# Optimization experiments

Measured on AMD Instinct MI355X. Metric: run time of the kernel, lower is better.

Reference implementation:

```python
import jax, jax.numpy as jnp
import numpy as np

TOP_K = 2

def setup_inputs() -> dict:
    key = jax.random.key(0)
    ks = jax.random.split(key, 5)
    B, S, H, F, E = 4, 512, 1024, 3584, 8
    x = jax.random.normal(ks[0], (B, S, H), dtype=jnp.float32)
    gate_w = jax.random.normal(ks[1], (H, E), dtype=jnp.float32) * (1.0 / np.sqrt(H))
    w1 = jax.random.normal(ks[2], (E, F, H), dtype=jnp.float32) * (1.0 / np.sqrt(H))
    w3 = jax.random.normal(ks[3], (E, F, H), dtype=jnp.float32) * (1.0 / np.sqrt(H))
    w2 = jax.random.normal(ks[4], (E, H, F), dtype=jnp.float32) * (1.0 / np.sqrt(F))
    return {"x": x, "gate_w": gate_w, "w1": w1, "w3": w3, "w2": w2}


def reference(x, gate_w, w1, w3, w2):
    # MoE top-2 routing (Mixtral-style), dense-dispatch formulation.
    B, S, H = x.shape
    E = gate_w.shape[1]
    xt = x.reshape(-1, H)                      # [T, H] flattened tokens
    T = xt.shape[0]
    logits = xt @ gate_w                       # [T, E] gate logits
    top_w, top_i = jax.lax.top_k(logits, TOP_K)    # [T, K]
    top_w = jax.nn.softmax(top_w, axis=-1)         # softmax over selected-k logits
    # combine[t, e] = routing weight of expert e for token t (0 if not selected)
    combine = jnp.zeros((T, E), dtype=xt.dtype)
    combine = combine.at[jnp.arange(T)[:, None], top_i].add(top_w)
    # SwiGLU experts: y_e = w2_e @ (silu(w1_e x) * (w3_e x))
    h = jnp.einsum('th,efh->tef', xt, w1)      # [T, E, F]
    g = jnp.einsum('th,efh->tef', xt, w3)      # [T, E, F]
    act = jax.nn.silu(h) * g                   # [T, E, F]
    out_e = jnp.einsum('tef,ehf->teh', act, w2)  # [T, E, H]
    out = jnp.einsum('teh,te->th', out_e, combine)  # weighted combine over experts
    return out.reshape(B, S, H)
```

## Files before the change

### kernel.cpp

```cpp
#include <hip/hip_runtime.h>
#include <hip/hip_bf16.h>
#include <stdint.h>

#define TOKENS 2048
#define HDIM 1024
#define FDIM 3584
#define NEXP 8
#define BK 32

typedef __attribute__((ext_vector_type(8))) short short8;
typedef __attribute__((ext_vector_type(4))) float floatx4;

#define AS1 __attribute__((address_space(1)))
#define AS3 __attribute__((address_space(3)))

__device__ __forceinline__ void glds16(const void* g, void* l) {
  __builtin_amdgcn_global_load_lds((const AS1 void*)g, (AS3 void*)l, 16, 0, 0);
}

__device__ __forceinline__ unsigned short f2bf(float f) {
  union { float f; unsigned int u; } c; c.f = f;
  unsigned int u = c.u;
  u += 0x7fffu + ((u >> 16) & 1u);
  return (unsigned short)(u >> 16);
}

__device__ __forceinline__ unsigned int pk2bf(float a, float b) {
  __hip_bfloat162 h = __float22bfloat162_rn(make_float2(a, b));
  union { __hip_bfloat162 h; unsigned int u; } c; c.h = h;
  return c.u;
}

__device__ __forceinline__ short8 pack_bf16(float4 c0, float4 c1) {
  union { short8 s; uint4 u; } o;
  o.u.x = pk2bf(c0.x, c0.y); o.u.y = pk2bf(c0.z, c0.w);
  o.u.z = pk2bf(c1.x, c1.y); o.u.w = pk2bf(c1.z, c1.w);
  return o.s;
}

__global__ void gate_kernel(const float* __restrict__ x,
                            const float* __restrict__ gw,
                            int* __restrict__ top_e,
                            float* __restrict__ top_w) {
  int wv = threadIdx.x >> 6;
  int lane = threadIdx.x & 63;
  int t = blockIdx.x * 4 + wv;
  if (t >= TOKENS) return;
  float p[NEXP];
#pragma unroll
  for (int e = 0; e < NEXP; e++) p[e] = 0.f;
  const float* xr = x + (size_t)t * HDIM;
  for (int h = lane; h < HDIM; h += 64) {
    float xv = xr[h];
    const float4* g4 = (const float4*)(gw + (size_t)h * NEXP);
    float4 a = g4[0], b = g4[1];
    p[0] += xv * a.x; p[1] += xv * a.y; p[2] += xv * a.z; p[3] += xv * a.w;
    p[4] += xv * b.x; p[5] += xv * b.y; p[6] += xv * b.z; p[7] += xv * b.w;
  }
#pragma unroll
  for (int e = 0; e < NEXP; e++) {
#pragma unroll
    for (int off = 32; off > 0; off >>= 1) p[e] += __shfl_xor(p[e], off, 64);
  }
  if (lane == 0) {
    int i0 = 0;
    for (int e = 1; e < NEXP; e++) if (p[e] > p[i0]) i0 = e;
    int i1 = (i0 == 0) ? 1 : 0;
    for (int e = 0; e < NEXP; e++) if (e != i0 && p[e] > p[i1]) i1 = e;
    float l0 = p[i0], l1 = p[i1];
    float e1 = __expf(l1 - l0);
    float s = 1.f + e1;
    top_e[t * 2] = i0; top_e[t * 2 + 1] = i1;
    top_w[t * 2] = 1.f / s; top_w[t * 2 + 1] = e1 / s;
  }
}

__global__ void route_kernel(const int* __restrict__ top_e,
                             int* __restrict__ count,
                             int* __restrict__ offs,
                             int* __restrict__ tok_of,
                             int* __restrict__ slot_of) {
  __shared__ int hist[NEXP];
  __shared__ int cur[NEXP];
  int tid = threadIdx.x;
  if (tid < NEXP) hist[tid] = 0;
  __syncthreads();
  int e[4];
#pragma unroll
  for (int j = 0; j < 4; j++) {
    int i = tid * 4 + j;
    e[j] = top_e[i];
    atomicAdd(&hist[e[j]], 1);
  }
  __syncthreads();
  if (tid == 0) {
    int o = 0;
    for (int k = 0; k < NEXP; k++) {
      offs[k] = o; cur[k] = o; count[k] = hist[k]; o += hist[k];
    }
  }
  __syncthreads();
#pragma unroll
  for (int j = 0; j < 4; j++) {
    int i = tid * 4 + j;
    int g = atomicAdd(&cur[e[j]], 1);
    tok_of[g] = i >> 1;
    slot_of[i] = g;
  }
}

__global__ void xconv_kernel(const float* __restrict__ x,
                             unsigned short* __restrict__ xbf) {
  int i = (blockIdx.x * blockDim.x + threadIdx.x) * 4;
  float4 v = *(const float4*)(x + i);
  uint2 pk;
  pk.x = pk2bf(v.x, v.y);
  pk.y = pk2bf(v.z, v.w);
  *(uint2*)(xbf + i) = pk;
}

#define G1_BM 128
#define G1_BF 64

__global__ __launch_bounds__(256, 3)
void gemm1_kernel(const unsigned short* __restrict__ xbf,
                  const float* __restrict__ w1,
                  const float* __restrict__ w3,
                  const int* __restrict__ count,
                  const int* __restrict__ offs,
                  const int* __restrict__ tok_of,
                  unsigned short* __restrict__ act) {
  int e = blockIdx.z;
  int cnt = count[e];
  int m0 = blockIdx.y * G1_BM;
  if (m0 >= cnt) return;
  int f0 = blockIdx.x * G1_BF;
  int off_e = offs[e];

  __shared__ __align__(16) unsigned short sA[2 * G1_BM * 32];
  __shared__ __align__(16) unsigned short sB1[2 * G1_BF * 32];
  __shared__ __align__(16) unsigned short sB3[2 * G1_BF * 32];

  int tid = threadIdx.x;
  int lane = tid & 63, wv = tid >> 6;

  const unsigned short* ag[2];
  char* alb[2];
#pragma unroll
  for (int p = 0; p < 2; p++) {
    int c = tid + p * 256;
    int row = c >> 2, slot = c & 3;
    int gch = slot ^ ((row >> 1) & 3);
    int r = m0 + row;
    int tok = tok_of[off_e + (r < cnt ? r : 0)];
    ag[p] = xbf + (size_t)tok * HDIM + gch * 8;
    alb[p] = (char*)sA + (wv * 64 + p * 256) * 16;
  }
  const float *b1g, *b3g;
  unsigned short *b1l, *b3l;
  {
    int row = tid >> 2, slot = tid & 3;
    int gch = slot ^ ((row >> 1) & 3);
    size_t wrow = (size_t)e * FDIM + f0 + row;
    b1g = w1 + wrow * HDIM + gch * 8;
    b3g = w3 + wrow * HDIM + gch * 8;
    b1l = sB1 + tid * 8;
    b3l = sB3 + tid * 8;
  }

  int lrow = lane & 15, quad = lane >> 4;
  int wm = wv >> 1, wn = wv & 1;

  floatx4 acc1[4][2], acc3[4][2];
#pragma unroll
  for (int i = 0; i < 4; i++)
#pragma unroll
    for (int j = 0; j < 2; j++) {
      acc1[i][j] = (floatx4){0.f, 0.f, 0.f, 0.f};
      acc3[i][j] = (floatx4){0.f, 0.f, 0.f, 0.f};
    }

  const int NT = HDIM / BK;

#pragma unroll
  for (int p = 0; p < 2; p++) glds16(ag[p], alb[p]);
  {
    float4 u0 = *(const float4*)(b1g);
    float4 u1 = *(const float4*)(b1g + 4);
    float4 v0 = *(const float4*)(b3g);
    float4 v1 = *(const float4*)(b3g + 4);
    *(short8*)b1l = pack_bf16(u0, u1);
    *(short8*)b3l = pack_bf16(v0, v1);
  }
  __syncthreads();

  int cur = 0;
  for (int t = 0; t < NT; t++) {
    int nb = cur ^ 1;
    float4 u0, u1, v0, v1;
    if (t + 1 < NT) {
      int k = (t + 1) * BK;
#pragma unroll
      for (int p = 0; p < 2; p++) glds16(ag[p] + k, alb[p] + nb * 8192);
      u0 = *(const float4*)(b1g + k);
      u1 = *(const float4*)(b1g + k + 4);
      v0 = *(const float4*)(b3g + k);
      v1 = *(const float4*)(b3g + k + 4);
    }

    const unsigned short* sAc = sA + cur * (G1_BM * 32);
    const unsigned short* sB1c = sB1 + cur * (G1_BF * 32);
    const unsigned short* sB3c = sB3 + cur * (G1_BF * 32);

    short8 af[4], b1f[2], b3f[2];
#pragma unroll
    for (int ms = 0; ms < 4; ms++) {
      int r = wm * 64 + ms * 16 + lrow;
      int sl = quad ^ ((r >> 1) & 3);
      af[ms] = *(const short8*)(sAc + r * 32 + sl * 8);
    }
#pragma unroll
    for (int ns = 0; ns < 2; ns++) {
      int r = wn * 32 + ns * 16 + lrow;
      int sl = quad ^ ((r >> 1) & 3);
      b1f[ns] = *(const short8*)(sB1c + r * 32 + sl * 8);
      b3f[ns] = *(const short8*)(sB3c + r * 32 + sl * 8);
    }
#pragma unroll
    for (int ms = 0; ms < 4; ms++)
#pragma unroll
      for (int ns = 0; ns < 2; ns++) {
        acc1[ms][ns] = __builtin_amdgcn_mfma_f32_16x16x32_bf16(af[ms], b1f[ns], acc1[ms][ns], 0, 0, 0);
        acc3[ms][ns] = __builtin_amdgcn_mfma_f32_16x16x32_bf16(af[ms], b3f[ns], acc3[ms][ns], 0, 0, 0);
      }

    if (t + 1 < NT) {
      *(short8*)(b1l + nb * (G1_BF * 32)) = pack_bf16(u0, u1);
      *(short8*)(b3l + nb * (G1_BF * 32)) = pack_bf16(v0, v1);
    }
    __syncthreads();
    cur = nb;
  }

#pragma unroll
  for (int ms = 0; ms < 4; ms++) {
#pragma unroll
    for (int reg = 0; reg < 4; reg++) {
      int slot = m0 + wm * 64 + ms * 16 + quad * 4 + reg;
      if (slot < cnt) {
        unsigned short* ar = act + (size_t)(off_e + slot) * FDIM + f0 + wn * 32;
#pragma unroll
        for (int ns = 0; ns < 2; ns++) {
          float h = acc1[ms][ns][reg];
          float g = acc3[ms][ns][reg];
          float a = h / (1.f + __expf(-h)) * g;
          ar[ns * 16 + lrow] = f2bf(a);
        }
      }
    }
  }
}

#define G2_BM 128
#define G2_BN 128
#define SPLITK 2
#define G2_KS (FDIM / SPLITK)

__global__ __launch_bounds__(256, 3)
void gemm2_kernel(const unsigned short* __restrict__ act,
                  const float* __restrict__ w2,
                  const int* __restrict__ count,
                  const int* __restrict__ offs,
                  float* __restrict__ part) {
  int zz = blockIdx.z;
  int e = zz & 7, sk = zz >> 3;
  int cnt = count[e];
  int m0 = blockIdx.y * G2_BM;
  if (m0 >= cnt) return;
  int h0 = blockIdx.x * G2_BN;
  int off_e = offs[e];
  int kb = sk * G2_KS;

  __shared__ __align__(16) unsigned short sA[2 * G2_BM * 32];
  __shared__ __align__(16) unsigned short sB[2 * G2_BN * 32];

  int tid = threadIdx.x;
  int lane = tid & 63, wv = tid >> 6;

  const unsigned short* ag[2];
  char* alb[2];
#pragma unroll
  for (int p = 0; p < 2; p++) {
    int c = tid + p * 256;
    int row = c >> 2, slot = c & 3;
    int gch = slot ^ ((row >> 1) & 3);
    int r = m0 + row;
    int rr = (r < cnt ? r : 0);
    ag[p] = act + (size_t)(off_e + rr) * FDIM + kb + gch * 8;
    alb[p] = (char*)sA + (wv * 64 + p * 256) * 16;
  }
  const float* bg[2];
  unsigned short* bl[2];
#pragma unroll
  for (int p = 0; p < 2; p++) {
    int c = tid + p * 256;
    int row = c >> 2, slot = c & 3;
    int gch = slot ^ ((row >> 1) & 3);
    bg[p] = w2 + ((size_t)e * HDIM + h0 + row) * FDIM + kb + gch * 8;
    bl[p] = sB + c * 8;
  }

  int lrow = lane & 15, quad = lane >> 4;
  int wm = wv >> 1, wn = wv & 1;

  floatx4 acc[4][4];
#pragma unroll
  for (int i = 0; i < 4; i++)
#pragma unroll
    for (int j = 0; j < 4; j++) acc[i][j] = (floatx4){0.f, 0.f, 0.f, 0.f};

  const int NT = G2_KS / BK;

#pragma unroll
  for (int p = 0; p < 2; p++) glds16(ag[p], alb[p]);
#pragma unroll
  for (int p = 0; p < 2; p++) {
    float4 u0 = *(const float4*)(bg[p]);
    float4 u1 = *(const float4*)(bg[p] + 4);
    *(short8*)(bl[p]) = pack_bf16(u0, u1);
  }
  __syncthreads();

  int cur = 0;
  for (int t = 0; t < NT; t++) {
    int nb = cur ^ 1;
    float4 u0[2], u1[2];
    if (t + 1 < NT) {
      int k = (t + 1) * BK;
#pragma unroll
      for (int p = 0; p < 2; p++) glds16(ag[p] + k, alb[p] + nb * 8192);
#pragma unroll
      for (int p = 0; p < 2; p++) {
        u0[p] = *(const float4*)(bg[p] + k);
        u1[p] = *(const float4*)(bg[p] + k + 4);
      }
    }

    const unsigned short* sAc = sA + cur * (G2_BM * 32);
    const unsigned short* sBc = sB + cur * (G2_BN * 32);

    short8 af[4], bf[4];
#pragma unroll
    for (int ms = 0; ms < 4; ms++) {
      int r = wm * 64 + ms * 16 + lrow;
      int sl = quad ^ ((r >> 1) & 3);
      af[ms] = *(const short8*)(sAc + r * 32 + sl * 8);
    }
#pragma unroll
    for (int ns = 0; ns < 4; ns++) {
      int r = wn * 64 + ns * 16 + lrow;
      int sl = quad ^ ((r >> 1) & 3);
      bf[ns] = *(const short8*)(sBc + r * 32 + sl * 8);
    }
#pragma unroll
    for (int ms = 0; ms < 4; ms++)
#pragma unroll
      for (int ns = 0; ns < 4; ns++)
        acc[ms][ns] = __builtin_amdgcn_mfma_f32_16x16x32_bf16(af[ms], bf[ns], acc[ms][ns], 0, 0, 0);

    if (t + 1 < NT) {
#pragma unroll
      for (int p = 0; p < 2; p++)
        *(short8*)(bl[p] + nb * (G2_BN * 32)) = pack_bf16(u0[p], u1[p]);
    }
    __syncthreads();
    cur = nb;
  }

#pragma unroll
  for (int ms = 0; ms < 4; ms++) {
#pragma unroll
    for (int reg = 0; reg < 4; reg++) {
      int slot = m0 + wm * 64 + ms * 16 + quad * 4 + reg;
      if (slot < cnt) {
        float* crow = part + ((size_t)sk * 4096 + off_e + slot) * HDIM + h0 + wn * 64;
#pragma unroll
        for (int ns = 0; ns < 4; ns++)
          crow[ns * 16 + lrow] = acc[ms][ns][reg];
      }
    }
  }
}

__global__ void combine_kernel(const float* __restrict__ part,
                               const int* __restrict__ slot_of,
                               const float* __restrict__ top_w,
                               float* __restrict__ out) {
  int t = blockIdx.x;
  int g0 = slot_of[t * 2], g1 = slot_of[t * 2 + 1];
  float w0 = top_w[t * 2], w1 = top_w[t * 2 + 1];
  int i = threadIdx.x;
  float4 s0 = {0.f, 0.f, 0.f, 0.f}, s1 = {0.f, 0.f, 0.f, 0.f};
#pragma unroll
  for (int sk = 0; sk < SPLITK; sk++) {
    float4 a = ((const float4*)(part + ((size_t)sk * 4096 + g0) * HDIM))[i];
    float4 b = ((const float4*)(part + ((size_t)sk * 4096 + g1) * HDIM))[i];
    s0.x += a.x; s0.y += a.y; s0.z += a.z; s0.w += a.w;
    s1.x += b.x; s1.y += b.y; s1.z += b.z; s1.w += b.w;
  }
  float4 r;
  r.x = w0 * s0.x + w1 * s1.x;
  r.y = w0 * s0.y + w1 * s1.y;
  r.z = w0 * s0.z + w1 * s1.z;
  r.w = w0 * s0.w + w1 * s1.w;
  ((float4*)(out + (size_t)t * HDIM))[i] = r;
}

extern "C" void kernel_launch(void* const* d_in, const int* in_sizes, int n_in,
                              void* d_out, int out_size, void* d_ws, size_t ws_size,
                              hipStream_t stream) {
  const float* x  = (const float*)d_in[0];
  const float* gw = (const float*)d_in[1];
  const float* w1 = (const float*)d_in[2];
  const float* w3 = (const float*)d_in[3];
  const float* w2 = (const float*)d_in[4];
  float* out = (float*)d_out;

  char* ws = (char*)d_ws;
  const size_t MB = 1ull << 20;
  float* top_w = (float*)(ws);
  int* top_e   = (int*)(ws + 16384);
  int* slot_of = (int*)(ws + 32768);
  int* tok_of  = (int*)(ws + 49152);
  int* count   = (int*)(ws + 65536);
  int* offs    = (int*)(ws + 65536 + 64);

  unsigned short* xbf = (unsigned short*)(ws + 1 * MB);
  unsigned short* act = (unsigned short*)(ws + 5 * MB);
  float* part = (float*)(ws + 35 * MB);

  gate_kernel<<<TOKENS / 4, 256, 0, stream>>>(x, gw, top_e, top_w);
  route_kernel<<<1, 1024, 0, stream>>>(top_e, count, offs, tok_of, slot_of);
  xconv_kernel<<<(TOKENS * HDIM) / (256 * 4), 256, 0, stream>>>(x, xbf);
  gemm1_kernel<<<dim3(FDIM / G1_BF, TOKENS / G1_BM, NEXP), 256, 0, stream>>>(
      xbf, w1, w3, count, offs, tok_of, act);
  gemm2_kernel<<<dim3(HDIM / G2_BN, TOKENS / G2_BM, NEXP * SPLITK), 256, 0, stream>>>(
      act, w2, count, offs, part);
  combine_kernel<<<TOKENS, 256, 0, stream>>>(part, slot_of, top_w, out);
}
```

Measured before the change: 508.2 us.

## Fuse x bf16 conversion into gate kernel and deepen B-operand prefetch

The fp32-to-bf16 conversion of x moves into the gate kernel, which already reads x, so one launch and one extra pass over x go away. Both expert GEMMs now prefetch the fp32 weight tile two K-steps ahead in registers and write the next tile's bf16 data to LDS before the MFMA loop instead of after it. This gives global weight loads more time to arrive. It also raises register pressure, which may lower occupancy under the launch bounds.

```diff
diff --git a/kernel.cpp b/kernel.cpp
--- a/kernel.cpp
+++ b/kernel.cpp
@@ -40,6 +40,7 @@
 
 __global__ void gate_kernel(const float* __restrict__ x,
                             const float* __restrict__ gw,
+                            unsigned short* __restrict__ xbf,
                             int* __restrict__ top_e,
                             float* __restrict__ top_w) {
   int wv = threadIdx.x >> 6;
@@ -50,12 +51,24 @@
 #pragma unroll
   for (int e = 0; e < NEXP; e++) p[e] = 0.f;
   const float* xr = x + (size_t)t * HDIM;
-  for (int h = lane; h < HDIM; h += 64) {
-    float xv = xr[h];
-    const float4* g4 = (const float4*)(gw + (size_t)h * NEXP);
-    float4 a = g4[0], b = g4[1];
-    p[0] += xv * a.x; p[1] += xv * a.y; p[2] += xv * a.z; p[3] += xv * a.w;
-    p[4] += xv * b.x; p[5] += xv * b.y; p[6] += xv * b.z; p[7] += xv * b.w;
+  unsigned short* xb = xbf + (size_t)t * HDIM;
+#pragma unroll
+  for (int it = 0; it < 4; it++) {
+    int h = it * 256 + lane * 4;
+    float4 v = *(const float4*)(xr + h);
+    uint2 pk;
+    pk.x = pk2bf(v.x, v.y);
+    pk.y = pk2bf(v.z, v.w);
+    *(uint2*)(xb + h) = pk;
+    const float* g0 = gw + (size_t)h * NEXP;
+#pragma unroll
+    for (int j = 0; j < 4; j++) {
+      float xv = (j == 0) ? v.x : (j == 1) ? v.y : (j == 2) ? v.z : v.w;
+      const float4* g4 = (const float4*)(g0 + j * NEXP);
+      float4 a = g4[0], b = g4[1];
+      p[0] += xv * a.x; p[1] += xv * a.y; p[2] += xv * a.z; p[3] += xv * a.w;
+      p[4] += xv * b.x; p[5] += xv * b.y; p[6] += xv * b.z; p[7] += xv * b.w;
+    }
   }
 #pragma unroll
   for (int e = 0; e < NEXP; e++) {
@@ -107,16 +120,6 @@
     tok_of[g] = i >> 1;
     slot_of[i] = g;
   }
-}
-
-__global__ void xconv_kernel(const float* __restrict__ x,
-                             unsigned short* __restrict__ xbf) {
-  int i = (blockIdx.x * blockDim.x + threadIdx.x) * 4;
-  float4 v = *(const float4*)(x + i);
-  uint2 pk;
-  pk.x = pk2bf(v.x, v.y);
-  pk.y = pk2bf(v.z, v.w);
-  *(uint2*)(xbf + i) = pk;
 }
 
 #define G1_BM 128
@@ -185,27 +188,31 @@
 #pragma unroll
   for (int p = 0; p < 2; p++) glds16(ag[p], alb[p]);
   {
-    float4 u0 = *(const float4*)(b1g);
-    float4 u1 = *(const float4*)(b1g + 4);
-    float4 v0 = *(const float4*)(b3g);
-    float4 v1 = *(const float4*)(b3g + 4);
-    *(short8*)b1l = pack_bf16(u0, u1);
-    *(short8*)b3l = pack_bf16(v0, v1);
-  }
+    float4 a0 = *(const float4*)(b1g), a1 = *(const float4*)(b1g + 4);
+    float4 c0 = *(const float4*)(b3g), c1 = *(const float4*)(b3g + 4);
+    *(short8*)b1l = pack_bf16(a0, a1);
+    *(short8*)b3l = pack_bf16(c0, c1);
+  }
+  float4 cu0 = *(const float4*)(b1g + BK), cu1 = *(const float4*)(b1g + BK + 4);
+  float4 cv0 = *(const float4*)(b3g + BK), cv1 = *(const float4*)(b3g + BK + 4);
   __syncthreads();
 
   int cur = 0;
   for (int t = 0; t < NT; t++) {
     int nb = cur ^ 1;
-    float4 u0, u1, v0, v1;
     if (t + 1 < NT) {
+      *(short8*)(b1l + nb * (G1_BF * 32)) = pack_bf16(cu0, cu1);
+      *(short8*)(b3l + nb * (G1_BF * 32)) = pack_bf16(cv0, cv1);
       int k = (t + 1) * BK;
 #pragma unroll
       for (int p = 0; p < 2; p++) glds16(ag[p] + k, alb[p] + nb * 8192);
-      u0 = *(const float4*)(b1g + k);
-      u1 = *(const float4*)(b1g + k + 4);
-      v0 = *(const float4*)(b3g + k);
-      v1 = *(const float4*)(b3g + k + 4);
+    }
+    float4 nu0 = {0.f, 0.f, 0.f, 0.f}, nu1 = {0.f, 0.f, 0.f, 0.f};
+    float4 nv0 = {0.f, 0.f, 0.f, 0.f}, nv1 = {0.f, 0.f, 0.f, 0.f};
+    if (t + 2 < NT) {
+      int k2 = (t + 2) * BK;
+      nu0 = *(const float4*)(b1g + k2); nu1 = *(const float4*)(b1g + k2 + 4);
+      nv0 = *(const float4*)(b3g + k2); nv1 = *(const float4*)(b3g + k2 + 4);
     }
 
     const unsigned short* sAc = sA + cur * (G1_BM * 32);
@@ -234,10 +241,7 @@
         acc3[ms][ns] = __builtin_amdgcn_mfma_f32_16x16x32_bf16(af[ms], b3f[ns], acc3[ms][ns], 0, 0, 0);
       }
 
-    if (t + 1 < NT) {
-      *(short8*)(b1l + nb * (G1_BF * 32)) = pack_bf16(u0, u1);
-      *(short8*)(b3l + nb * (G1_BF * 32)) = pack_bf16(v0, v1);
-    }
+    cu0 = nu0; cu1 = nu1; cv0 = nv0; cv1 = nv1;
     __syncthreads();
     cur = nb;
   }
@@ -325,24 +329,41 @@
   for (int p = 0; p < 2; p++) glds16(ag[p], alb[p]);
 #pragma unroll
   for (int p = 0; p < 2; p++) {
-    float4 u0 = *(const float4*)(bg[p]);
-    float4 u1 = *(const float4*)(bg[p] + 4);
-    *(short8*)(bl[p]) = pack_bf16(u0, u1);
+    float4 a0 = *(const float4*)(bg[p]);
+    float4 a1 = *(const float4*)(bg[p] + 4);
+    *(short8*)(bl[p]) = pack_bf16(a0, a1);
+  }
+  float4 cu0[2], cu1[2];
+#pragma unroll
+  for (int p = 0; p < 2; p++) {
+    cu0[p] = *(const float4*)(bg[p] + BK);
+    cu1[p] = *(const float4*)(bg[p] + BK + 4);
   }
   __syncthreads();
 
   int cur = 0;
   for (int t = 0; t < NT; t++) {
     int nb = cur ^ 1;
-    float4 u0[2], u1[2];
     if (t + 1 < NT) {
+#pragma unroll
+      for (int p = 0; p < 2; p++)
+        *(short8*)(bl[p] + nb * (G2_BN * 32)) = pack_bf16(cu0[p], cu1[p]);
       int k = (t + 1) * BK;
 #pragma unroll
       for (int p = 0; p < 2; p++) glds16(ag[p] + k, alb[p] + nb * 8192);
+    }
+    float4 nu0[2], nu1[2];
+#pragma unroll
+    for (int p = 0; p < 2; p++) {
+      nu0[p] = (float4){0.f, 0.f, 0.f, 0.f};
+      nu1[p] = (float4){0.f, 0.f, 0.f, 0.f};
+    }
+    if (t + 2 < NT) {
+      int k2 = (t + 2) * BK;
 #pragma unroll
       for (int p = 0; p < 2; p++) {
-        u0[p] = *(const float4*)(bg[p] + k);
-        u1[p] = *(const float4*)(bg[p] + k + 4);
+        nu0[p] = *(const float4*)(bg[p] + k2);
+        nu1[p] = *(const float4*)(bg[p] + k2 + 4);
       }
     }
 
@@ -368,11 +389,8 @@
       for (int ns = 0; ns < 4; ns++)
         acc[ms][ns] = __builtin_amdgcn_mfma_f32_16x16x32_bf16(af[ms], bf[ns], acc[ms][ns], 0, 0, 0);
 
-    if (t + 1 < NT) {
-#pragma unroll
-      for (int p = 0; p < 2; p++)
-        *(short8*)(bl[p] + nb * (G2_BN * 32)) = pack_bf16(u0[p], u1[p]);
-    }
+#pragma unroll
+    for (int p = 0; p < 2; p++) { cu0[p] = nu0[p]; cu1[p] = nu1[p]; }
     __syncthreads();
     cur = nb;
   }
@@ -439,9 +457,8 @@
   unsigned short* act = (unsigned short*)(ws + 5 * MB);
   float* part = (float*)(ws + 35 * MB);
 
-  gate_kernel<<<TOKENS / 4, 256, 0, stream>>>(x, gw, top_e, top_w);
+  gate_kernel<<<TOKENS / 4, 256, 0, stream>>>(x, gw, xbf, top_e, top_w);
   route_kernel<<<1, 1024, 0, stream>>>(top_e, count, offs, tok_of, slot_of);
-  xconv_kernel<<<(TOKENS * HDIM) / (256 * 4), 256, 0, stream>>>(x, xbf);
   gemm1_kernel<<<dim3(FDIM / G1_BF, TOKENS / G1_BM, NEXP), 256, 0, stream>>>(
       xbf, w1, w3, count, offs, tok_of, act);
   gemm2_kernel<<<dim3(HDIM / G2_BN, TOKENS / G2_BM, NEXP * SPLITK), 256, 0, stream>>>(
```

After: 475.3 us. 6.5% less time.
